# Kernel optimization log

Measured on AMD Instinct MI355X. Metric: run time of the kernel, lower is better.

Reference implementation:

```python
import jax, jax.numpy as jnp
import numpy as np

DIM = 2048
N_HEADS = 32
N_KV_HEADS = 8
HEAD_DIM = DIM // N_HEADS  # 64
N_REP = N_HEADS // N_KV_HEADS  # 4
B, S = 1, 2048


def _rope(t, cos, sin):
    # t: (b, s, h, head_dim); cos/sin: (s, head_dim//2)
    tr = t.reshape(*t.shape[:-1], -1, 2)
    a, b = tr[..., 0], tr[..., 1]
    c = cos[None, :, None, :]
    s_ = sin[None, :, None, :]
    ra = a * c - b * s_
    rb = a * s_ + b * c
    return jnp.stack([ra, rb], axis=-1).reshape(t.shape)


def setup_inputs() -> dict:
    key = jax.random.key(0)
    ks = jax.random.split(key, 6)
    sc = 1.0 / np.sqrt(DIM)
    x = jax.random.normal(ks[0], (B, S, DIM), dtype=jnp.float32)
    wq = jax.random.normal(ks[1], (DIM, N_HEADS * HEAD_DIM), dtype=jnp.float32) * sc
    wk = jax.random.normal(ks[2], (DIM, N_KV_HEADS * HEAD_DIM), dtype=jnp.float32) * sc
    wv = jax.random.normal(ks[3], (DIM, N_KV_HEADS * HEAD_DIM), dtype=jnp.float32) * sc
    wo = jax.random.normal(ks[4], (N_HEADS * HEAD_DIM, DIM), dtype=jnp.float32) * sc
    # rotary frequencies (theta = 500000 as in Llama3)
    inv = 1.0 / (500000.0 ** (np.arange(0, HEAD_DIM, 2, dtype=np.float32) / HEAD_DIM))
    ang = np.arange(S, dtype=np.float32)[:, None] * inv[None, :]
    freqs_cos = jnp.asarray(np.cos(ang), dtype=jnp.float32)
    freqs_sin = jnp.asarray(np.sin(ang), dtype=jnp.float32)
    # causal additive mask
    mask = jnp.triu(jnp.full((S, S), -1e9, dtype=jnp.float32), k=1)
    return {"x": x, "wq": wq, "wk": wk, "wv": wv, "wo": wo,
            "freqs_cos": freqs_cos, "freqs_sin": freqs_sin, "mask": mask,
            "start_pos": 0}


def reference(x, wq, wk, wv, wo, freqs_cos, freqs_sin, mask, start_pos):
    b, s, _ = x.shape
    xq = (x @ wq).reshape(b, s, N_HEADS, HEAD_DIM)
    xk = (x @ wk).reshape(b, s, N_KV_HEADS, HEAD_DIM)
    xv = (x @ wv).reshape(b, s, N_KV_HEADS, HEAD_DIM)
    xq = _rope(xq, freqs_cos, freqs_sin)
    xk = _rope(xk, freqs_cos, freqs_sin)
    # GQA without repeat_interleave: view queries as (b, s, kv, rep, d)
    q = xq.reshape(b, s, N_KV_HEADS, N_REP, HEAD_DIM)
    scale = 1.0 / np.sqrt(HEAD_DIM)
    # scores: (b, kv, rep, q, k)
    scores = jnp.einsum('bqkrd,bskd->bkrqs', q, xk) * scale
    scores = scores + mask[None, None, None, :, :]
    probs = jax.nn.softmax(scores.astype(jnp.float32), axis=-1).astype(x.dtype)
    out = jnp.einsum('bkrqs,bskd->bqkrd', probs, xv)
    out = out.reshape(b, s, N_HEADS * HEAD_DIM)
    return out @ wo
```

## Files before the change

### kernel.cpp

```cpp
#include <hip/hip_runtime.h>
#include <hip/hip_bf16.h>

#define DIM 2048
#define S_LEN 2048
#define N_HEADS 32
#define N_KV_HEADS 8
#define HEAD_DIM 64
#define KV_DIM (N_KV_HEADS * HEAD_DIM)
#define QKV_N (DIM + 2 * KV_DIM)
#define QSCALE 0.18033688011112042f

typedef __attribute__((ext_vector_type(8))) short bf16x8;
typedef __attribute__((ext_vector_type(4))) float f32x4;

__device__ __forceinline__ unsigned short bf16_of(float f) {
    __hip_bfloat16 h = __float2bfloat16(f);
    return *reinterpret_cast<unsigned short*>(&h);
}
__device__ __forceinline__ float f_of_bf16(unsigned short u) {
    unsigned int x = ((unsigned int)u) << 16;
    return __uint_as_float(x);
}
__device__ __forceinline__ void gl_lds16(const void* g, void* l) {
    __builtin_amdgcn_global_load_lds((const __attribute__((address_space(1))) void*)g,
                                     (__attribute__((address_space(3))) void*)l, 16, 0, 0);
}
__device__ __forceinline__ unsigned int pack2tr(float lo, float hi) {
    return __builtin_amdgcn_perm(__float_as_uint(hi), __float_as_uint(lo), 0x07060302u);
}
__device__ __forceinline__ float max3f(float a, float b, float c) {
    float d;
    asm("v_max3_f32 %0, %1, %2, %3" : "=v"(d) : "v"(a), "v"(b), "v"(c));
    return d;
}

__global__ __launch_bounds__(256) void prep(const float* __restrict__ x,
                                            const float* __restrict__ wq,
                                            const float* __restrict__ wk,
                                            const float* __restrict__ wv,
                                            const float* __restrict__ wo,
                                            unsigned short* __restrict__ xbf,
                                            unsigned short* __restrict__ wqkvT,
                                            unsigned short* __restrict__ woT) {
    __shared__ float tile[64][65];
    const int t = threadIdx.x;
    int b = blockIdx.x;
    if (b < 4096) {
        int idx = b * 256 + t;
        float4 f = ((const float4*)x)[idx];
        ushort4 u;
        u.x = bf16_of(f.x); u.y = bf16_of(f.y); u.z = bf16_of(f.z); u.w = bf16_of(f.w);
        ((ushort4*)xbf)[idx] = u;
        return;
    }
    b -= 4096;
    const float* src;
    unsigned short* dst;
    int src_cols, bx, by;
    if (b < 1024)      { src = wq; dst = wqkvT;                                src_cols = DIM;    bx = b & 31;          by = b >> 5; }
    else if (b < 1280) { src = wk; dst = wqkvT + (size_t)DIM * DIM;            src_cols = KV_DIM; bx = (b - 1024) & 7;  by = (b - 1024) >> 3; }
    else if (b < 1536) { src = wv; dst = wqkvT + (size_t)(DIM + KV_DIM) * DIM; src_cols = KV_DIM; bx = (b - 1280) & 7;  by = (b - 1280) >> 3; }
    else               { src = wo; dst = woT;                                  src_cols = DIM;    bx = (b - 1536) & 31; by = (b - 1536) >> 5; }
    const int c0 = bx * 64, r0 = by * 64;
#pragma unroll
    for (int i = 0; i < 4; i++) {
        int idx = t + i * 256;
        int r = idx >> 4, c4 = (idx & 15) * 4;
        float4 f = *(const float4*)&src[(size_t)(r0 + r) * src_cols + c0 + c4];
        tile[r][c4 + 0] = f.x; tile[r][c4 + 1] = f.y;
        tile[r][c4 + 2] = f.z; tile[r][c4 + 3] = f.w;
    }
    __syncthreads();
#pragma unroll
    for (int i = 0; i < 4; i++) {
        int idx = t + i * 256;
        int rr = idx >> 4, cc = (idx & 15) * 4;
        ushort4 u;
        u.x = bf16_of(tile[cc + 0][rr]);
        u.y = bf16_of(tile[cc + 1][rr]);
        u.z = bf16_of(tile[cc + 2][rr]);
        u.w = bf16_of(tile[cc + 3][rr]);
        *(ushort4*)&dst[(size_t)(c0 + rr) * DIM + r0 + cc] = u;
    }
}

__global__ __launch_bounds__(256) void gemm_bt64(const unsigned short* __restrict__ A,
                                                 const unsigned short* __restrict__ Bt,
                                                 void* __restrict__ Cv,
                                                 int M, int N, int K, int c_bf16) {
    __shared__ unsigned short As[2][128 * 64];
    __shared__ unsigned short Bs[2][64 * 64];
    const int tid = threadIdx.x;
    const int wave = tid >> 6, lane = tid & 63;
    const int m16 = lane & 15, quad = lane >> 4;
    const int m0 = blockIdx.y * 128, n0 = blockIdx.x * 64;
    const int wm = (wave >> 1) * 64, wn = (wave & 1) * 32;

    const int lrow = lane >> 3;
    const int gc = (lane & 7) ^ lrow;
    const unsigned short* Ab = A + (size_t)(m0 + wave * 8 + lrow) * K + gc * 8;
    const unsigned short* Bb = Bt + (size_t)(n0 + wave * 8 + lrow) * K + gc * 8;

    f32x4 acc[4][2];
#pragma unroll
    for (int mb = 0; mb < 4; mb++)
#pragma unroll
        for (int nb = 0; nb < 2; nb++) acc[mb][nb] = (f32x4){0.f, 0.f, 0.f, 0.f};

#pragma unroll
    for (int g = 0; g < 4; g++)
        gl_lds16(Ab + (size_t)g * 32 * K, &As[0][(g * 32 + wave * 8) * 64]);
#pragma unroll
    for (int g = 0; g < 2; g++)
        gl_lds16(Bb + (size_t)g * 32 * K, &Bs[0][(g * 32 + wave * 8) * 64]);

    const int nt = K >> 6;
    for (int kt = 0; kt < nt; kt++) {
        __syncthreads();
        if (kt + 1 < nt) {
            const int nb2 = (kt + 1) & 1;
            const int k0 = (kt + 1) << 6;
#pragma unroll
            for (int g = 0; g < 4; g++)
                gl_lds16(Ab + (size_t)g * 32 * K + k0, &As[nb2][(g * 32 + wave * 8) * 64]);
#pragma unroll
            for (int g = 0; g < 2; g++)
                gl_lds16(Bb + (size_t)g * 32 * K + k0, &Bs[nb2][(g * 32 + wave * 8) * 64]);
        }
        const unsigned short* A_ = As[kt & 1];
        const unsigned short* B_ = Bs[kt & 1];
#pragma unroll
        for (int ks = 0; ks < 2; ks++) {
            const int ch = (ks * 4 + quad) ^ (m16 & 7);
            bf16x8 af[4], bfr[2];
#pragma unroll
            for (int mb = 0; mb < 4; mb++)
                af[mb] = *(const bf16x8*)&A_[(wm + mb * 16 + m16) * 64 + ch * 8];
#pragma unroll
            for (int nb = 0; nb < 2; nb++)
                bfr[nb] = *(const bf16x8*)&B_[(wn + nb * 16 + m16) * 64 + ch * 8];
#pragma unroll
            for (int mb = 0; mb < 4; mb++)
#pragma unroll
                for (int nb = 0; nb < 2; nb++)
                    acc[mb][nb] = __builtin_amdgcn_mfma_f32_16x16x32_bf16(af[mb], bfr[nb], acc[mb][nb], 0, 0, 0);
        }
    }

    if (c_bf16) {
        unsigned short* C = (unsigned short*)Cv;
#pragma unroll
        for (int mb = 0; mb < 4; mb++)
#pragma unroll
            for (int nb = 0; nb < 2; nb++)
#pragma unroll
                for (int r = 0; r < 4; r++)
                    C[(size_t)(m0 + wm + mb * 16 + quad * 4 + r) * N + n0 + wn + nb * 16 + m16] =
                        bf16_of(acc[mb][nb][r]);
    } else {
        float* C = (float*)Cv;
#pragma unroll
        for (int mb = 0; mb < 4; mb++)
#pragma unroll
            for (int nb = 0; nb < 2; nb++)
#pragma unroll
                for (int r = 0; r < 4; r++)
                    C[(size_t)(m0 + wm + mb * 16 + quad * 4 + r) * N + n0 + wn + nb * 16 + m16] =
                        acc[mb][nb][r];
    }
}

__global__ __launch_bounds__(256) void rope_kv(const unsigned short* __restrict__ qkv,
                                               unsigned short* __restrict__ kbf,
                                               unsigned short* __restrict__ vbt,
                                               const float* __restrict__ fcos,
                                               const float* __restrict__ fsin) {
    __shared__ unsigned short tile[64][65];
    const int t = threadIdx.x;
    int b = blockIdx.x;
    if (b < 512) {
        int idx = b * 256 + t;
        int s = idx >> 6;
        int rem = idx & 63;
        int hh = rem >> 3, j = rem & 7;
        int srcoff = s * QKV_N + DIM + hh * 64 + j * 8;
        int dstoff = s * KV_DIM + hh * 64 + j * 8;
        bf16x8 v8 = *(const bf16x8*)&qkv[srcoff];
        float4 c4 = *(const float4*)&fcos[s * 32 + j * 4];
        float4 s4 = *(const float4*)&fsin[s * 32 + j * 4];
        float cs[4] = {c4.x, c4.y, c4.z, c4.w};
        float sn[4] = {s4.x, s4.y, s4.z, s4.w};
        bf16x8 o;
#pragma unroll
        for (int p = 0; p < 4; p++) {
            float a = f_of_bf16((unsigned short)v8[2 * p]);
            float bb = f_of_bf16((unsigned short)v8[2 * p + 1]);
            o[2 * p]     = (short)bf16_of(a * cs[p] - bb * sn[p]);
            o[2 * p + 1] = (short)bf16_of(a * sn[p] + bb * cs[p]);
        }
        *(bf16x8*)&kbf[dstoff] = o;
        return;
    }
    b -= 512;
    const int d0 = (b & 7) * 64;
    const int s0 = (b >> 3) * 64;
#pragma unroll
    for (int i = 0; i < 16; i++) {
        int idx = t + i * 256;
        int r = idx >> 6, c = idx & 63;
        tile[r][c] = qkv[(size_t)(s0 + r) * QKV_N + DIM + KV_DIM + d0 + c];
    }
    __syncthreads();
#pragma unroll
    for (int i = 0; i < 16; i++) {
        int idx = t + i * 256;
        int r = idx >> 6, c = idx & 63;
        int key = s0 + c;
        int kl = key & 127;
        int kp = (kl & 0x60) | ((kl & 0x0C) << 1) | ((kl & 0x10) >> 2) | (kl & 3);
        vbt[(size_t)(d0 + r) * S_LEN + (key & ~127) + kp] = tile[c][r];
    }
}

__global__ __launch_bounds__(256) void attn_mfma9(const unsigned short* __restrict__ qkv,
                                                  const unsigned short* __restrict__ kb,
                                                  const unsigned short* __restrict__ vbt,
                                                  const float* __restrict__ fcos,
                                                  const float* __restrict__ fsin,
                                                  unsigned short* __restrict__ out) {
    const int h  = blockIdx.x;
    const int qt = 31 - (int)blockIdx.y;
    const int kh = h >> 2;
    const int tid  = threadIdx.x;
    const int wave = tid >> 6;
    const int lane = tid & 63;
    const int m16  = lane & 15;
    const int quad = lane >> 4;

    __shared__ unsigned short Ks[2][128 * 64];
    __shared__ unsigned short Vt[64 * 128];

    const int lrow8 = lane >> 3;
    const int kc    = (lane & 7) ^ lrow8;
    const int lrow4 = lane >> 4;
    const int vc    = (lane & 15) ^ ((wave * 4 + lrow4) & 7);

    const unsigned short* Kbase = kb + (size_t)kh * 64 + (size_t)(wave * 8 + lrow8) * KV_DIM + kc * 8;
    const unsigned short* Vbase = vbt + (size_t)(kh * 64 + wave * 4 + lrow4) * S_LEN + vc * 8;

    bf16x8 ones;
#pragma unroll
    for (int i = 0; i < 8; i++) ones[i] = (short)0x3F80;

    const int q0 = qt * 64;
    const int n_iter = (qt >> 1) + 1;

    bf16x8 qa[2];
    {
        const int qrow = q0 + wave * 16 + m16;
        const unsigned short* qsrc = qkv + (size_t)qrow * QKV_N + h * 64;
#pragma unroll
        for (int ks = 0; ks < 2; ks++) {
            bf16x8 raw = *(const bf16x8*)&qsrc[ks * 32 + quad * 8];
            float4 c4 = *(const float4*)&fcos[qrow * 32 + ks * 16 + quad * 4];
            float4 s4 = *(const float4*)&fsin[qrow * 32 + ks * 16 + quad * 4];
            float cs[4] = {c4.x, c4.y, c4.z, c4.w};
            float sn[4] = {s4.x, s4.y, s4.z, s4.w};
#pragma unroll
            for (int p = 0; p < 4; p++) {
                float a = f_of_bf16((unsigned short)raw[2 * p]);
                float bb = f_of_bf16((unsigned short)raw[2 * p + 1]);
                qa[ks][2 * p]     = (short)bf16_of((a * cs[p] - bb * sn[p]) * QSCALE);
                qa[ks][2 * p + 1] = (short)bf16_of((a * sn[p] + bb * cs[p]) * QSCALE);
            }
        }
    }

    f32x4 o_acc[4];
#pragma unroll
    for (int nb = 0; nb < 4; nb++) o_acc[nb] = (f32x4){0.f, 0.f, 0.f, 0.f};
    f32x4 l_acc = (f32x4){0.f, 0.f, 0.f, 0.f};
    float m_s = -1e30f;
    const int qrow_lane = q0 + wave * 16 + m16;
    const int orow_base = q0 + wave * 16 + quad * 4;

#pragma unroll
    for (int g = 0; g < 4; g++)
        gl_lds16(Kbase + (size_t)(g * 32) * KV_DIM, &Ks[0][(g * 32 + wave * 8) * 64]);

    for (int kt = 0; kt < n_iter; kt++) {
        asm volatile("s_waitcnt vmcnt(0)" ::: "memory");
        __builtin_amdgcn_s_barrier();
        __builtin_amdgcn_sched_barrier(0);

        const int knext = (kt + 1 < n_iter) ? (kt + 1) : kt;
#pragma unroll
        for (int g = 0; g < 4; g++)
            gl_lds16(Vbase + (size_t)g * 16 * S_LEN + kt * 128,
                     &Vt[(g * 16 + wave * 4) * 128]);
#pragma unroll
        for (int g = 0; g < 4; g++)
            gl_lds16(Kbase + (size_t)(knext * 128 + g * 32) * KV_DIM,
                     &Ks[(kt + 1) & 1][(g * 32 + wave * 8) * 64]);

        const unsigned short* K_ = Ks[kt & 1];

        f32x4 sc[8];
#pragma unroll
        for (int cb = 0; cb < 8; cb++) sc[cb] = (f32x4){0.f, 0.f, 0.f, 0.f};
        __builtin_amdgcn_s_setprio(1);
#pragma unroll
        for (int ks = 0; ks < 2; ks++) {
            const int slot = (ks * 4 + quad) ^ (m16 & 7);
#pragma unroll
            for (int cb = 0; cb < 8; cb++) {
                bf16x8 kf = *(const bf16x8*)&K_[(cb * 16 + m16) * 64 + slot * 8];
                sc[cb] = __builtin_amdgcn_mfma_f32_16x16x32_bf16(kf, qa[ks], sc[cb], 0, 0, 0);
            }
        }
        __builtin_amdgcn_s_setprio(0);

        if (kt == n_iter - 1) {
#pragma unroll
            for (int cb = 0; cb < 8; cb++) {
                int key = kt * 128 + cb * 16 + quad * 4;
#pragma unroll
                for (int r = 0; r < 4; r++)
                    if (key + r > qrow_lane) sc[cb][r] = -1e30f;
            }
        }

        float rmax = fmaxf(sc[0][0], sc[0][1]);
        rmax = max3f(sc[0][2], sc[0][3], rmax);
#pragma unroll
        for (int cb = 1; cb < 8; cb++) {
            rmax = max3f(sc[cb][0], sc[cb][1], rmax);
            rmax = max3f(sc[cb][2], sc[cb][3], rmax);
        }
        rmax = fmaxf(rmax, __shfl_xor(rmax, 16, 64));
        rmax = fmaxf(rmax, __shfl_xor(rmax, 32, 64));

        if (!__all(rmax - m_s <= 8.0f)) {
            float mnew = fmaxf(m_s, rmax);
            float alpha = __builtin_amdgcn_exp2f(m_s - mnew);
            m_s = mnew;
#pragma unroll
            for (int r = 0; r < 4; r++) {
                float a_r = __shfl(alpha, quad * 4 + r, 64);
#pragma unroll
                for (int nb = 0; nb < 4; nb++) o_acc[nb][r] *= a_r;
                l_acc[r] *= a_r;
            }
        }

#pragma unroll
        for (int cb = 0; cb < 8; cb++)
#pragma unroll
            for (int r = 0; r < 4; r++)
                sc[cb][r] = __builtin_amdgcn_exp2f(sc[cb][r] - m_s);

        unsigned int P01[8], P23[8];
#pragma unroll
        for (int cb = 0; cb < 8; cb++) {
            P01[cb] = pack2tr(sc[cb][0], sc[cb][1]);
            P23[cb] = pack2tr(sc[cb][2], sc[cb][3]);
        }

        asm volatile("s_waitcnt vmcnt(4)" ::: "memory");
        __builtin_amdgcn_s_barrier();
        __builtin_amdgcn_sched_barrier(0);

        __builtin_amdgcn_s_setprio(1);
#pragma unroll
        for (int ks = 0; ks < 4; ks++) {
            union { unsigned int u[4]; bf16x8 v; } pa;
            pa.u[0] = P01[2 * ks];     pa.u[1] = P23[2 * ks];
            pa.u[2] = P01[2 * ks + 1]; pa.u[3] = P23[2 * ks + 1];
            const int slot = (ks * 4 + quad) ^ (m16 & 7);
#pragma unroll
            for (int nb = 0; nb < 4; nb++) {
                bf16x8 vf = *(const bf16x8*)&Vt[(nb * 16 + m16) * 128 + slot * 8];
                o_acc[nb] = __builtin_amdgcn_mfma_f32_16x16x32_bf16(pa.v, vf, o_acc[nb], 0, 0, 0);
            }
            l_acc = __builtin_amdgcn_mfma_f32_16x16x32_bf16(pa.v, ones, l_acc, 0, 0, 0);
        }
        __builtin_amdgcn_s_setprio(0);
    }

#pragma unroll
    for (int r = 0; r < 4; r++) {
        float inv_l = 1.f / l_acc[r];
#pragma unroll
        for (int nb = 0; nb < 4; nb++)
            out[(size_t)(orow_base + r) * DIM + h * 64 + nb * 16 + m16] =
                bf16_of(o_acc[nb][r] * inv_l);
    }
}

extern "C" void kernel_launch(void* const* d_in, const int* in_sizes, int n_in,
                              void* d_out, int out_size, void* d_ws, size_t ws_size,
                              hipStream_t stream) {
    const float* x    = (const float*)d_in[0];
    const float* wq   = (const float*)d_in[1];
    const float* wk   = (const float*)d_in[2];
    const float* wv   = (const float*)d_in[3];
    const float* wo   = (const float*)d_in[4];
    const float* fcos = (const float*)d_in[5];
    const float* fsin = (const float*)d_in[6];

    char* ws = (char*)d_ws;
    const size_t MB = 1024 * 1024;
    unsigned short* xbf    = (unsigned short*)(ws);
    unsigned short* wqkvT  = (unsigned short*)(ws + 8 * MB);
    unsigned short* woT    = (unsigned short*)(ws + 20 * MB);
    unsigned short* qkvbf  = (unsigned short*)(ws + 28 * MB);
    unsigned short* vbt    = (unsigned short*)(ws + 40 * MB);
    unsigned short* kbf    = (unsigned short*)(ws + 16 * MB);
    unsigned short* attnbf = (unsigned short*)(ws);

    prep<<<4096 + 2560, 256, 0, stream>>>(x, wq, wk, wv, wo, xbf, wqkvT, woT);

    gemm_bt64<<<dim3(QKV_N / 64, S_LEN / 128), 256, 0, stream>>>(xbf, wqkvT, qkvbf,
                                                                 S_LEN, QKV_N, DIM, 1);

    rope_kv<<<512 + 256, 256, 0, stream>>>(qkvbf, kbf, vbt, fcos, fsin);

    attn_mfma9<<<dim3(N_HEADS, 32), 256, 0, stream>>>(qkvbf, kbf, vbt, fcos, fsin, attnbf);

    gemm_bt64<<<dim3(DIM / 64, S_LEN / 128), 256, 0, stream>>>(attnbf, woT, d_out,
                                                               S_LEN, DIM, DIM, 0);
}
```

Before: 215.9 us.

## Process 128 query rows per attention block with two Q sub-tiles per wave

Each attention block now covers 128 query rows instead of 64, and each wave holds two 16-row Q fragments that share every K and V fragment loaded from LDS. This halves the number of blocks and the K/V global-to-LDS traffic per query, and removes the half-wasted causal tiles of the previous 64-row scheme. The grid order is also changed, scheduling the longest tiles of the first half first and then the short tiles ascending. In exchange, register pressure roughly doubles for scores and accumulators, and the grid drops to 512 blocks, which may lower occupancy and load balance.

Result: slower. 240.2 us (+11.2%).

```diff
diff --git a/kernel.cpp b/kernel.cpp
--- a/kernel.cpp
+++ b/kernel.cpp
@@ -222,14 +222,15 @@
     }
 }
 
-__global__ __launch_bounds__(256) void attn_mfma9(const unsigned short* __restrict__ qkv,
-                                                  const unsigned short* __restrict__ kb,
-                                                  const unsigned short* __restrict__ vbt,
-                                                  const float* __restrict__ fcos,
-                                                  const float* __restrict__ fsin,
-                                                  unsigned short* __restrict__ out) {
+__global__ __launch_bounds__(256) void attn_mfma10(const unsigned short* __restrict__ qkv,
+                                                   const unsigned short* __restrict__ kb,
+                                                   const unsigned short* __restrict__ vbt,
+                                                   const float* __restrict__ fcos,
+                                                   const float* __restrict__ fsin,
+                                                   unsigned short* __restrict__ out) {
     const int h  = blockIdx.x;
-    const int qt = 31 - (int)blockIdx.y;
+    const int y  = blockIdx.y;
+    const int qt = (y < 8) ? (15 - y) : (y - 8);
     const int kh = h >> 2;
     const int tid  = threadIdx.x;
     const int wave = tid >> 6;
@@ -252,12 +253,13 @@
 #pragma unroll
     for (int i = 0; i < 8; i++) ones[i] = (short)0x3F80;
 
-    const int q0 = qt * 64;
-    const int n_iter = (qt >> 1) + 1;
-
-    bf16x8 qa[2];
-    {
-        const int qrow = q0 + wave * 16 + m16;
+    const int q0 = qt * 128;
+    const int n_iter = qt + 1;
+
+    bf16x8 qa[2][2];
+#pragma unroll
+    for (int s = 0; s < 2; s++) {
+        const int qrow = q0 + wave * 32 + s * 16 + m16;
         const unsigned short* qsrc = qkv + (size_t)qrow * QKV_N + h * 64;
 #pragma unroll
         for (int ks = 0; ks < 2; ks++) {
@@ -270,19 +272,19 @@
             for (int p = 0; p < 4; p++) {
                 float a = f_of_bf16((unsigned short)raw[2 * p]);
                 float bb = f_of_bf16((unsigned short)raw[2 * p + 1]);
-                qa[ks][2 * p]     = (short)bf16_of((a * cs[p] - bb * sn[p]) * QSCALE);
-                qa[ks][2 * p + 1] = (short)bf16_of((a * sn[p] + bb * cs[p]) * QSCALE);
-            }
-        }
-    }
-
-    f32x4 o_acc[4];
-#pragma unroll
-    for (int nb = 0; nb < 4; nb++) o_acc[nb] = (f32x4){0.f, 0.f, 0.f, 0.f};
-    f32x4 l_acc = (f32x4){0.f, 0.f, 0.f, 0.f};
-    float m_s = -1e30f;
-    const int qrow_lane = q0 + wave * 16 + m16;
-    const int orow_base = q0 + wave * 16 + quad * 4;
+                qa[s][ks][2 * p]     = (short)bf16_of((a * cs[p] - bb * sn[p]) * QSCALE);
+                qa[s][ks][2 * p + 1] = (short)bf16_of((a * sn[p] + bb * cs[p]) * QSCALE);
+            }
+        }
+    }
+
+    f32x4 o_acc[2][4];
+#pragma unroll
+    for (int s = 0; s < 2; s++)
+#pragma unroll
+        for (int nb = 0; nb < 4; nb++) o_acc[s][nb] = (f32x4){0.f, 0.f, 0.f, 0.f};
+    f32x4 l_acc[2] = {(f32x4){0.f, 0.f, 0.f, 0.f}, (f32x4){0.f, 0.f, 0.f, 0.f}};
+    float m_s[2] = {-1e30f, -1e30f};
 
 #pragma unroll
     for (int g = 0; g < 4; g++)
@@ -305,9 +307,11 @@
 
         const unsigned short* K_ = Ks[kt & 1];
 
-        f32x4 sc[8];
-#pragma unroll
-        for (int cb = 0; cb < 8; cb++) sc[cb] = (f32x4){0.f, 0.f, 0.f, 0.f};
+        f32x4 sc[2][8];
+#pragma unroll
+        for (int s = 0; s < 2; s++)
+#pragma unroll
+            for (int cb = 0; cb < 8; cb++) sc[s][cb] = (f32x4){0.f, 0.f, 0.f, 0.f};
         __builtin_amdgcn_s_setprio(1);
 #pragma unroll
         for (int ks = 0; ks < 2; ks++) {
@@ -315,55 +319,63 @@
 #pragma unroll
             for (int cb = 0; cb < 8; cb++) {
                 bf16x8 kf = *(const bf16x8*)&K_[(cb * 16 + m16) * 64 + slot * 8];
-                sc[cb] = __builtin_amdgcn_mfma_f32_16x16x32_bf16(kf, qa[ks], sc[cb], 0, 0, 0);
+                sc[0][cb] = __builtin_amdgcn_mfma_f32_16x16x32_bf16(kf, qa[0][ks], sc[0][cb], 0, 0, 0);
+                sc[1][cb] = __builtin_amdgcn_mfma_f32_16x16x32_bf16(kf, qa[1][ks], sc[1][cb], 0, 0, 0);
             }
         }
         __builtin_amdgcn_s_setprio(0);
 
         if (kt == n_iter - 1) {
 #pragma unroll
+            for (int s = 0; s < 2; s++) {
+                const int qrl = q0 + wave * 32 + s * 16 + m16;
+#pragma unroll
+                for (int cb = 0; cb < 8; cb++) {
+                    int key = kt * 128 + cb * 16 + quad * 4;
+#pragma unroll
+                    for (int r = 0; r < 4; r++)
+                        if (key + r > qrl) sc[s][cb][r] = -1e30f;
+                }
+            }
+        }
+
+        unsigned int P01[2][8], P23[2][8];
+#pragma unroll
+        for (int s = 0; s < 2; s++) {
+            float rmax = fmaxf(sc[s][0][0], sc[s][0][1]);
+            rmax = max3f(sc[s][0][2], sc[s][0][3], rmax);
+#pragma unroll
+            for (int cb = 1; cb < 8; cb++) {
+                rmax = max3f(sc[s][cb][0], sc[s][cb][1], rmax);
+                rmax = max3f(sc[s][cb][2], sc[s][cb][3], rmax);
+            }
+            rmax = fmaxf(rmax, __shfl_xor(rmax, 16, 64));
+            rmax = fmaxf(rmax, __shfl_xor(rmax, 32, 64));
+
+            if (!__all(rmax - m_s[s] <= 8.0f)) {
+                float mnew = fmaxf(m_s[s], rmax);
+                float alpha = __builtin_amdgcn_exp2f(m_s[s] - mnew);
+                m_s[s] = mnew;
+#pragma unroll
+                for (int r = 0; r < 4; r++) {
+                    float a_r = __shfl(alpha, quad * 4 + r, 64);
+#pragma unroll
+                    for (int nb = 0; nb < 4; nb++) o_acc[s][nb][r] *= a_r;
+                    l_acc[s][r] *= a_r;
+                }
+            }
+
+#pragma unroll
+            for (int cb = 0; cb < 8; cb++)
+#pragma unroll
+                for (int r = 0; r < 4; r++)
+                    sc[s][cb][r] = __builtin_amdgcn_exp2f(sc[s][cb][r] - m_s[s]);
+
+#pragma unroll
             for (int cb = 0; cb < 8; cb++) {
-                int key = kt * 128 + cb * 16 + quad * 4;
-#pragma unroll
-                for (int r = 0; r < 4; r++)
-                    if (key + r > qrow_lane) sc[cb][r] = -1e30f;
-            }
-        }
-
-        float rmax = fmaxf(sc[0][0], sc[0][1]);
-        rmax = max3f(sc[0][2], sc[0][3], rmax);
-#pragma unroll
-        for (int cb = 1; cb < 8; cb++) {
-            rmax = max3f(sc[cb][0], sc[cb][1], rmax);
-            rmax = max3f(sc[cb][2], sc[cb][3], rmax);
-        }
-        rmax = fmaxf(rmax, __shfl_xor(rmax, 16, 64));
-        rmax = fmaxf(rmax, __shfl_xor(rmax, 32, 64));
-
-        if (!__all(rmax - m_s <= 8.0f)) {
-            float mnew = fmaxf(m_s, rmax);
-            float alpha = __builtin_amdgcn_exp2f(m_s - mnew);
-            m_s = mnew;
-#pragma unroll
-            for (int r = 0; r < 4; r++) {
-                float a_r = __shfl(alpha, quad * 4 + r, 64);
-#pragma unroll
-                for (int nb = 0; nb < 4; nb++) o_acc[nb][r] *= a_r;
-                l_acc[r] *= a_r;
-            }
-        }
-
-#pragma unroll
-        for (int cb = 0; cb < 8; cb++)
-#pragma unroll
-            for (int r = 0; r < 4; r++)
-                sc[cb][r] = __builtin_amdgcn_exp2f(sc[cb][r] - m_s);
-
-        unsigned int P01[8], P23[8];
-#pragma unroll
-        for (int cb = 0; cb < 8; cb++) {
-            P01[cb] = pack2tr(sc[cb][0], sc[cb][1]);
-            P23[cb] = pack2tr(sc[cb][2], sc[cb][3]);
+                P01[s][cb] = pack2tr(sc[s][cb][0], sc[s][cb][1]);
+                P23[s][cb] = pack2tr(sc[s][cb][2], sc[s][cb][3]);
+            }
         }
 
         asm volatile("s_waitcnt vmcnt(4)" ::: "memory");
@@ -373,27 +385,35 @@
         __builtin_amdgcn_s_setprio(1);
 #pragma unroll
         for (int ks = 0; ks < 4; ks++) {
-            union { unsigned int u[4]; bf16x8 v; } pa;
-            pa.u[0] = P01[2 * ks];     pa.u[1] = P23[2 * ks];
-            pa.u[2] = P01[2 * ks + 1]; pa.u[3] = P23[2 * ks + 1];
+            union { unsigned int u[4]; bf16x8 v; } pa0, pa1;
+            pa0.u[0] = P01[0][2 * ks];     pa0.u[1] = P23[0][2 * ks];
+            pa0.u[2] = P01[0][2 * ks + 1]; pa0.u[3] = P23[0][2 * ks + 1];
+            pa1.u[0] = P01[1][2 * ks];     pa1.u[1] = P23[1][2 * ks];
+            pa1.u[2] = P01[1][2 * ks + 1]; pa1.u[3] = P23[1][2 * ks + 1];
             const int slot = (ks * 4 + quad) ^ (m16 & 7);
 #pragma unroll
             for (int nb = 0; nb < 4; nb++) {
                 bf16x8 vf = *(const bf16x8*)&Vt[(nb * 16 + m16) * 128 + slot * 8];
-                o_acc[nb] = __builtin_amdgcn_mfma_f32_16x16x32_bf16(pa.v, vf, o_acc[nb], 0, 0, 0);
-            }
-            l_acc = __builtin_amdgcn_mfma_f32_16x16x32_bf16(pa.v, ones, l_acc, 0, 0, 0);
+                o_acc[0][nb] = __builtin_amdgcn_mfma_f32_16x16x32_bf16(pa0.v, vf, o_acc[0][nb], 0, 0, 0);
+                o_acc[1][nb] = __builtin_amdgcn_mfma_f32_16x16x32_bf16(pa1.v, vf, o_acc[1][nb], 0, 0, 0);
+            }
+            l_acc[0] = __builtin_amdgcn_mfma_f32_16x16x32_bf16(pa0.v, ones, l_acc[0], 0, 0, 0);
+            l_acc[1] = __builtin_amdgcn_mfma_f32_16x16x32_bf16(pa1.v, ones, l_acc[1], 0, 0, 0);
         }
         __builtin_amdgcn_s_setprio(0);
     }
 
 #pragma unroll
-    for (int r = 0; r < 4; r++) {
-        float inv_l = 1.f / l_acc[r];
-#pragma unroll
-        for (int nb = 0; nb < 4; nb++)
-            out[(size_t)(orow_base + r) * DIM + h * 64 + nb * 16 + m16] =
-                bf16_of(o_acc[nb][r] * inv_l);
+    for (int s = 0; s < 2; s++) {
+        const int ob = q0 + wave * 32 + s * 16 + quad * 4;
+#pragma unroll
+        for (int r = 0; r < 4; r++) {
+            float inv_l = 1.f / l_acc[s][r];
+#pragma unroll
+            for (int nb = 0; nb < 4; nb++)
+                out[(size_t)(ob + r) * DIM + h * 64 + nb * 16 + m16] =
+                    bf16_of(o_acc[s][nb][r] * inv_l);
+        }
     }
 }
 
@@ -425,7 +445,7 @@
 
     rope_kv<<<512 + 256, 256, 0, stream>>>(qkvbf, kbf, vbt, fcos, fsin);
 
-    attn_mfma9<<<dim3(N_HEADS, 32), 256, 0, stream>>>(qkvbf, kbf, vbt, fcos, fsin, attnbf);
+    attn_mfma10<<<dim3(N_HEADS, 16), 256, 0, stream>>>(qkvbf, kbf, vbt, fcos, fsin, attnbf);
 
     gemm_bt64<<<dim3(DIM / 64, S_LEN / 128), 256, 0, stream>>>(attnbf, woT, d_out,
                                                                S_LEN, DIM, DIM, 0);
```

## Fuse K RoPE and V transpose into QKV GEMM epilogue

Applied to the files above, without the earlier changes.

Removes the separate rope_kv kernel by applying rotary embedding to K columns and writing V in transposed, permuted layout directly from the QKV GEMM accumulators. This saves a kernel launch and a round trip of K/V through global memory. The kbf buffer is relocated so it no longer overlaps the weight buffer being read concurrently. The epilogue now issues scattered 2-byte K stores and strided V stores, which may be less coalesced than the old tiled transpose.

After: 213.9 us. Within noise of the previous version (-0.9%).

```diff
diff --git a/kernel.cpp b/kernel.cpp
--- a/kernel.cpp
+++ b/kernel.cpp
@@ -87,7 +87,11 @@
 __global__ __launch_bounds__(256) void gemm_bt64(const unsigned short* __restrict__ A,
                                                  const unsigned short* __restrict__ Bt,
                                                  void* __restrict__ Cv,
-                                                 int M, int N, int K, int c_bf16) {
+                                                 unsigned short* __restrict__ kbf,
+                                                 unsigned short* __restrict__ vbt,
+                                                 const float* __restrict__ fcos,
+                                                 const float* __restrict__ fsin,
+                                                 int M, int N, int K, int mode) {
     __shared__ unsigned short As[2][128 * 64];
     __shared__ unsigned short Bs[2][64 * 64];
     const int tid = threadIdx.x;
@@ -147,7 +151,17 @@
         }
     }
 
-    if (c_bf16) {
+    if (mode == 0) {
+        float* C = (float*)Cv;
+#pragma unroll
+        for (int mb = 0; mb < 4; mb++)
+#pragma unroll
+            for (int nb = 0; nb < 2; nb++)
+#pragma unroll
+                for (int r = 0; r < 4; r++)
+                    C[(size_t)(m0 + wm + mb * 16 + quad * 4 + r) * N + n0 + wn + nb * 16 + m16] =
+                        acc[mb][nb][r];
+    } else if (n0 < DIM) {
         unsigned short* C = (unsigned short*)Cv;
 #pragma unroll
         for (int mb = 0; mb < 4; mb++)
@@ -157,68 +171,41 @@
                 for (int r = 0; r < 4; r++)
                     C[(size_t)(m0 + wm + mb * 16 + quad * 4 + r) * N + n0 + wn + nb * 16 + m16] =
                         bf16_of(acc[mb][nb][r]);
+    } else if (n0 < DIM + KV_DIM) {
+        const int even = !(m16 & 1);
+#pragma unroll
+        for (int mb = 0; mb < 4; mb++)
+#pragma unroll
+            for (int nb = 0; nb < 2; nb++) {
+                const int khd  = n0 - DIM + wn + nb * 16 + m16;
+                const int pair = ((wn + nb * 16 + m16) & 63) >> 1;
+#pragma unroll
+                for (int r = 0; r < 4; r++) {
+                    const int s = m0 + wm + mb * 16 + quad * 4 + r;
+                    float v = acc[mb][nb][r];
+                    float p = __shfl_xor(v, 1, 64);
+                    float c  = fcos[s * 32 + pair];
+                    float sn = fsin[s * 32 + pair];
+                    float res = even ? (v * c - p * sn) : (v * c + p * sn);
+                    kbf[(size_t)s * KV_DIM + khd] = bf16_of(res);
+                }
+            }
     } else {
-        float* C = (float*)Cv;
 #pragma unroll
         for (int mb = 0; mb < 4; mb++)
 #pragma unroll
-            for (int nb = 0; nb < 2; nb++)
-#pragma unroll
-                for (int r = 0; r < 4; r++)
-                    C[(size_t)(m0 + wm + mb * 16 + quad * 4 + r) * N + n0 + wn + nb * 16 + m16] =
-                        acc[mb][nb][r];
-    }
-}
-
-__global__ __launch_bounds__(256) void rope_kv(const unsigned short* __restrict__ qkv,
-                                               unsigned short* __restrict__ kbf,
-                                               unsigned short* __restrict__ vbt,
-                                               const float* __restrict__ fcos,
-                                               const float* __restrict__ fsin) {
-    __shared__ unsigned short tile[64][65];
-    const int t = threadIdx.x;
-    int b = blockIdx.x;
-    if (b < 512) {
-        int idx = b * 256 + t;
-        int s = idx >> 6;
-        int rem = idx & 63;
-        int hh = rem >> 3, j = rem & 7;
-        int srcoff = s * QKV_N + DIM + hh * 64 + j * 8;
-        int dstoff = s * KV_DIM + hh * 64 + j * 8;
-        bf16x8 v8 = *(const bf16x8*)&qkv[srcoff];
-        float4 c4 = *(const float4*)&fcos[s * 32 + j * 4];
-        float4 s4 = *(const float4*)&fsin[s * 32 + j * 4];
-        float cs[4] = {c4.x, c4.y, c4.z, c4.w};
-        float sn[4] = {s4.x, s4.y, s4.z, s4.w};
-        bf16x8 o;
-#pragma unroll
-        for (int p = 0; p < 4; p++) {
-            float a = f_of_bf16((unsigned short)v8[2 * p]);
-            float bb = f_of_bf16((unsigned short)v8[2 * p + 1]);
-            o[2 * p]     = (short)bf16_of(a * cs[p] - bb * sn[p]);
-            o[2 * p + 1] = (short)bf16_of(a * sn[p] + bb * cs[p]);
-        }
-        *(bf16x8*)&kbf[dstoff] = o;
-        return;
-    }
-    b -= 512;
-    const int d0 = (b & 7) * 64;
-    const int s0 = (b >> 3) * 64;
-#pragma unroll
-    for (int i = 0; i < 16; i++) {
-        int idx = t + i * 256;
-        int r = idx >> 6, c = idx & 63;
-        tile[r][c] = qkv[(size_t)(s0 + r) * QKV_N + DIM + KV_DIM + d0 + c];
-    }
-    __syncthreads();
-#pragma unroll
-    for (int i = 0; i < 16; i++) {
-        int idx = t + i * 256;
-        int r = idx >> 6, c = idx & 63;
-        int key = s0 + c;
-        int kl = key & 127;
-        int kp = (kl & 0x60) | ((kl & 0x0C) << 1) | ((kl & 0x10) >> 2) | (kl & 3);
-        vbt[(size_t)(d0 + r) * S_LEN + (key & ~127) + kp] = tile[c][r];
+            for (int nb = 0; nb < 2; nb++) {
+                const int d = n0 - DIM - KV_DIM + wn + nb * 16 + m16;
+                const int sbase = m0 + wm + mb * 16 + quad * 4;
+                const int kl = sbase & 127;
+                const int kpb = (kl & 0x60) | ((kl & 0x0C) << 1) | ((kl & 0x10) >> 2);
+                ushort4 u;
+                u.x = bf16_of(acc[mb][nb][0]);
+                u.y = bf16_of(acc[mb][nb][1]);
+                u.z = bf16_of(acc[mb][nb][2]);
+                u.w = bf16_of(acc[mb][nb][3]);
+                *(ushort4*)&vbt[(size_t)d * S_LEN + (sbase & ~127) + kpb] = u;
+            }
     }
 }
 
@@ -415,18 +402,16 @@
     unsigned short* woT    = (unsigned short*)(ws + 20 * MB);
     unsigned short* qkvbf  = (unsigned short*)(ws + 28 * MB);
     unsigned short* vbt    = (unsigned short*)(ws + 40 * MB);
-    unsigned short* kbf    = (unsigned short*)(ws + 16 * MB);
+    unsigned short* kbf    = (unsigned short*)(ws + 42 * MB);
     unsigned short* attnbf = (unsigned short*)(ws);
 
     prep<<<4096 + 2560, 256, 0, stream>>>(x, wq, wk, wv, wo, xbf, wqkvT, woT);
 
-    gemm_bt64<<<dim3(QKV_N / 64, S_LEN / 128), 256, 0, stream>>>(xbf, wqkvT, qkvbf,
-                                                                 S_LEN, QKV_N, DIM, 1);
-
-    rope_kv<<<512 + 256, 256, 0, stream>>>(qkvbf, kbf, vbt, fcos, fsin);
+    gemm_bt64<<<dim3(QKV_N / 64, S_LEN / 128), 256, 0, stream>>>(
+        xbf, wqkvT, qkvbf, kbf, vbt, fcos, fsin, S_LEN, QKV_N, DIM, 2);
 
     attn_mfma9<<<dim3(N_HEADS, 32), 256, 0, stream>>>(qkvbf, kbf, vbt, fcos, fsin, attnbf);
 
-    gemm_bt64<<<dim3(DIM / 64, S_LEN / 128), 256, 0, stream>>>(attnbf, woT, d_out,
-                                                               S_LEN, DIM, DIM, 0);
-}
+    gemm_bt64<<<dim3(DIM / 64, S_LEN / 128), 256, 0, stream>>>(
+        attnbf, woT, d_out, nullptr, nullptr, nullptr, nullptr, S_LEN, DIM, DIM, 0);
+}
```
